# Kernel optimization log

Measured on AMD Instinct MI355X. Metric: run time of the kernel, lower is better.

## Reference

```python
import jax, jax.numpy as jnp
import numpy as np

EPS = 1e-5
V, D, S, B, H, DH, FF, LE, LD = 32000, 512, 1024, 2, 8, 64, 2048, 2, 2


def _ln(x, g, b):
    m = x.mean(-1, keepdims=True)
    v = ((x - m) ** 2).mean(-1, keepdims=True)
    return (x - m) * jax.lax.rsqrt(v + EPS) * g + b


def _mha(qi, ki, vi, wq, wk, wv, uw, ub, mask):
    # wq/wk/wv: [H, D, DH] stacked per-head no-bias projections (concat order == head order)
    q = jnp.einsum('bsd,hde->bhse', qi, wq)
    k = jnp.einsum('btd,hde->bhte', ki, wk)
    v = jnp.einsum('btd,hde->bhte', vi, wv)
    scale = float(wq.shape[-1]) ** 0.5  # FAITHFUL to source: scores are MULTIPLIED by sqrt(d_head)
    s = jnp.einsum('bhse,bhte->bhst', q, k) * scale
    s = jnp.where(mask, s, -jnp.inf)  # causal tril mask applied in every attention (incl. cross)
    a = jax.nn.softmax(s, axis=-1)
    o = jnp.einsum('bhst,bhte->bhse', a, v)
    b_, h_, s_, e_ = o.shape
    o = o.transpose(0, 2, 1, 3).reshape(b_, s_, h_ * e_)
    return o @ uw + ub


def _posenc(seq, d):
    pos = jnp.arange(seq, dtype=jnp.float32)[:, None]
    den = jnp.exp(jnp.arange(0, d, 2, dtype=jnp.float32) * (-np.log(10000.0) / d))
    pe = jnp.zeros((seq, d), jnp.float32)
    pe = pe.at[:, 0::2].set(jnp.sin(pos * den))
    pe = pe.at[:, 1::2].set(jnp.cos(pos * den))
    return pe


def _forward(tokens, emb, enc_wq, enc_wk, enc_wv, enc_uo_w, enc_uo_b,
             enc_ln1_g, enc_ln1_b, enc_ln2_g, enc_ln2_b,
             enc_ff_w1, enc_ff_b1, enc_ff_w2, enc_ff_b2,
             dec_sa_wq, dec_sa_wk, dec_sa_wv, dec_sa_uo_w, dec_sa_uo_b,
             dec_ca_wq, dec_ca_wk, dec_ca_wv, dec_ca_uo_w, dec_ca_uo_b,
             dec_ln1_g, dec_ln1_b, dec_ln2_g, dec_ln2_b, dec_ln3_g, dec_ln3_b,
             dec_ff_w1, dec_ff_b1, dec_ff_w2, dec_ff_b2,
             ln_enc_g, ln_enc_b, ln_dec_g, ln_dec_b, head_w, head_b):
    b, s = tokens.shape
    d = emb.shape[1]
    x = emb[tokens] + _posenc(s, d)  # [B, S, D]
    mask = jnp.tril(jnp.ones((s, s), bool))
    enc = jax.lax.stop_gradient(x)  # source: x.detach().clone()
    for l in range(enc_wq.shape[0]):
        h = _ln(enc, enc_ln1_g[l], enc_ln1_b[l])
        enc = enc + _mha(h, h, h, enc_wq[l], enc_wk[l], enc_wv[l], enc_uo_w[l], enc_uo_b[l], mask)
        h = _ln(enc, enc_ln2_g[l], enc_ln2_b[l])
        enc = enc + (jnp.maximum(h @ enc_ff_w1[l] + enc_ff_b1[l], 0.0) @ enc_ff_w2[l] + enc_ff_b2[l])
    enc = _ln(enc, ln_enc_g, ln_enc_b)
    for l in range(dec_sa_wq.shape[0]):
        h = _ln(x, dec_ln1_g[l], dec_ln1_b[l])
        x = x + _mha(h, h, h, dec_sa_wq[l], dec_sa_wk[l], dec_sa_wv[l], dec_sa_uo_w[l], dec_sa_uo_b[l], mask)
        h = _ln(x, dec_ln2_g[l], dec_ln2_b[l])
        x = x + _mha(h, enc, enc, dec_ca_wq[l], dec_ca_wk[l], dec_ca_wv[l], dec_ca_uo_w[l], dec_ca_uo_b[l], mask)
        h = _ln(x, dec_ln3_g[l], dec_ln3_b[l])
        x = x + (jnp.maximum(h @ dec_ff_w1[l] + dec_ff_b1[l], 0.0) @ dec_ff_w2[l] + dec_ff_b2[l])
    x = _ln(x, ln_dec_g, ln_dec_b)
    return x @ head_w + head_b  # [B, S, V]


def setup_inputs():
    key = jax.random.key(0)
    ks = iter(jax.random.split(key, 64))
    def n(shape):
        return jax.random.normal(next(ks), shape, jnp.float32) * 0.02
    return {
        'tokens': jax.random.randint(next(ks), (B, S), 0, V, jnp.int32),
        'emb': n((V, D)),
        'enc_wq': n((LE, H, D, DH)), 'enc_wk': n((LE, H, D, DH)), 'enc_wv': n((LE, H, D, DH)),
        'enc_uo_w': n((LE, D, D)), 'enc_uo_b': jnp.zeros((LE, D), jnp.float32),
        'enc_ln1_g': jnp.ones((LE, D), jnp.float32), 'enc_ln1_b': jnp.zeros((LE, D), jnp.float32),
        'enc_ln2_g': jnp.ones((LE, D), jnp.float32), 'enc_ln2_b': jnp.zeros((LE, D), jnp.float32),
        'enc_ff_w1': n((LE, D, FF)), 'enc_ff_b1': jnp.zeros((LE, FF), jnp.float32),
        'enc_ff_w2': n((LE, FF, D)), 'enc_ff_b2': jnp.zeros((LE, D), jnp.float32),
        'dec_sa_wq': n((LD, H, D, DH)), 'dec_sa_wk': n((LD, H, D, DH)), 'dec_sa_wv': n((LD, H, D, DH)),
        'dec_sa_uo_w': n((LD, D, D)), 'dec_sa_uo_b': jnp.zeros((LD, D), jnp.float32),
        'dec_ca_wq': n((LD, H, D, DH)), 'dec_ca_wk': n((LD, H, D, DH)), 'dec_ca_wv': n((LD, H, D, DH)),
        'dec_ca_uo_w': n((LD, D, D)), 'dec_ca_uo_b': jnp.zeros((LD, D), jnp.float32),
        'dec_ln1_g': jnp.ones((LD, D), jnp.float32), 'dec_ln1_b': jnp.zeros((LD, D), jnp.float32),
        'dec_ln2_g': jnp.ones((LD, D), jnp.float32), 'dec_ln2_b': jnp.zeros((LD, D), jnp.float32),
        'dec_ln3_g': jnp.ones((LD, D), jnp.float32), 'dec_ln3_b': jnp.zeros((LD, D), jnp.float32),
        'dec_ff_w1': n((LD, D, FF)), 'dec_ff_b1': jnp.zeros((LD, FF), jnp.float32),
        'dec_ff_w2': n((LD, FF, D)), 'dec_ff_b2': jnp.zeros((LD, D), jnp.float32),
        'ln_enc_g': jnp.ones((D,), jnp.float32), 'ln_enc_b': jnp.zeros((D,), jnp.float32),
        'ln_dec_g': jnp.ones((D,), jnp.float32), 'ln_dec_b': jnp.zeros((D,), jnp.float32),
        'head_w': n((D, V)), 'head_b': jnp.zeros((V,), jnp.float32),
    }


def reference(tokens, emb, enc_wq, enc_wk, enc_wv, enc_uo_w, enc_uo_b,
              enc_ln1_g, enc_ln1_b, enc_ln2_g, enc_ln2_b,
              enc_ff_w1, enc_ff_b1, enc_ff_w2, enc_ff_b2,
              dec_sa_wq, dec_sa_wk, dec_sa_wv, dec_sa_uo_w, dec_sa_uo_b,
              dec_ca_wq, dec_ca_wk, dec_ca_wv, dec_ca_uo_w, dec_ca_uo_b,
              dec_ln1_g, dec_ln1_b, dec_ln2_g, dec_ln2_b, dec_ln3_g, dec_ln3_b,
              dec_ff_w1, dec_ff_b1, dec_ff_w2, dec_ff_b2,
              ln_enc_g, ln_enc_b, ln_dec_g, ln_dec_b, head_w, head_b):
    return _forward(tokens, emb, enc_wq, enc_wk, enc_wv, enc_uo_w, enc_uo_b,
                    enc_ln1_g, enc_ln1_b, enc_ln2_g, enc_ln2_b,
                    enc_ff_w1, enc_ff_b1, enc_ff_w2, enc_ff_b2,
                    dec_sa_wq, dec_sa_wk, dec_sa_wv, dec_sa_uo_w, dec_sa_uo_b,
                    dec_ca_wq, dec_ca_wk, dec_ca_wv, dec_ca_uo_w, dec_ca_uo_b,
                    dec_ln1_g, dec_ln1_b, dec_ln2_g, dec_ln2_b, dec_ln3_g, dec_ln3_b,
                    dec_ff_w1, dec_ff_b1, dec_ff_w2, dec_ff_b2,
                    ln_enc_g, ln_enc_b, ln_dec_g, ln_dec_b, head_w, head_b)
```

## Files before the change

### kernel.cpp

```cpp
#include <hip/hip_runtime.h>
#include <cstddef>
#include <cstdint>

constexpr int Vv = 32000, Dd = 512, Ss = 1024, Bb = 2, Hh = 8, DHd = 64, FFf = 2048;
constexpr int Tt = Bb * Ss;
constexpr int QKVW = 3 * Dd;
constexpr float EPSf = 1e-5f;

typedef unsigned short ushort_t;
typedef short bf16x8 __attribute__((ext_vector_type(8)));
typedef short short4v __attribute__((ext_vector_type(4)));
typedef float f32x4 __attribute__((ext_vector_type(4)));

constexpr size_t AQKV = 0;
constexpr size_t AUO  = 4718592;
constexpr size_t AFF1 = 6291456;
constexpr size_t AFF2 = 10485760;
constexpr size_t AEND = 14680064;

__device__ __forceinline__ ushort_t f2b(float f) {
  unsigned int u = __float_as_uint(f);
  unsigned int r = (u + 0x7FFFu + ((u >> 16) & 1u)) >> 16;
  return (ushort_t)r;
}
__device__ __forceinline__ float bits2f(ushort_t u) {
  return __uint_as_float((unsigned int)u << 16);
}

__device__ __forceinline__ void st_out(float* p, float v) { *p = v; }
__device__ __forceinline__ void st_out(ushort_t* p, float v) { *p = f2b(v); }

__device__ __forceinline__ void gload_lds16(const void* g, void* l) {
  __builtin_amdgcn_global_load_lds(
      (const __attribute__((address_space(1))) unsigned int*)g,
      (__attribute__((address_space(3))) unsigned int*)l, 16, 0, 0);
}

__global__ __launch_bounds__(256) void embed_pe_k(const int* __restrict__ tok,
                                                  const float* __restrict__ emb,
                                                  float* __restrict__ X,
                                                  float* __restrict__ ENC) {
  int row = blockIdx.x;
  int s = row & (Ss - 1);
  int t = tok[row];
  const float* e = emb + (size_t)t * Dd;
  for (int d = threadIdx.x; d < Dd; d += 256) {
    int i = d >> 1;
    float den = expf(-(float)(2 * i) * (9.210340371976184f / 512.0f));
    float ang = (float)s * den;
    float pe = (d & 1) ? cosf(ang) : sinf(ang);
    float v = e[d] + pe;
    X[(size_t)row * Dd + d] = v;
    ENC[(size_t)row * Dd + d] = v;
  }
}

__global__ __launch_bounds__(256) void layernorm_k(const float* __restrict__ in,
                                                   const float* __restrict__ g,
                                                   const float* __restrict__ b,
                                                   ushort_t* __restrict__ out) {
  int row = blockIdx.x;
  const float* x = in + (size_t)row * Dd;
  int tid = threadIdx.x;
  float v0 = x[tid], v1 = x[tid + 256];
  float s = v0 + v1, ss = v0 * v0 + v1 * v1;
  for (int o = 32; o; o >>= 1) {
    s  += __shfl_down(s, o, 64);
    ss += __shfl_down(ss, o, 64);
  }
  __shared__ float rs[4], rss[4];
  int wid = tid >> 6, lane = tid & 63;
  if (lane == 0) { rs[wid] = s; rss[wid] = ss; }
  __syncthreads();
  __shared__ float mean_s, inv_s;
  if (tid == 0) {
    float a = rs[0] + rs[1] + rs[2] + rs[3];
    float c = rss[0] + rss[1] + rss[2] + rss[3];
    float m = a / Dd;
    float var = c / Dd - m * m;
    mean_s = m;
    inv_s = rsqrtf(var + EPSf);
  }
  __syncthreads();
  float m = mean_s, inv = inv_s;
  out[(size_t)row * Dd + tid]       = f2b((v0 - m) * inv * g[tid]       + b[tid]);
  out[(size_t)row * Dd + tid + 256] = f2b((v1 - m) * inv * g[tid + 256] + b[tid + 256]);
}

__global__ __launch_bounds__(256) void prep_all_k(
    const float* __restrict__ ewq, const float* __restrict__ ewk, const float* __restrict__ ewv,
    const float* __restrict__ swq, const float* __restrict__ swk, const float* __restrict__ swv,
    const float* __restrict__ cwq, const float* __restrict__ cwk, const float* __restrict__ cwv,
    const float* __restrict__ euo, const float* __restrict__ suo, const float* __restrict__ cuo,
    const float* __restrict__ eff1, const float* __restrict__ dff1,
    const float* __restrict__ eff2, const float* __restrict__ dff2,
    ushort_t* __restrict__ arena) {
  const float* src;
  ushort_t* dst;
  int R, C, tile;
  int idx = blockIdx.x;
  if (idx < 4608) {
    tile = idx & 31;
    int rest = idx >> 5;
    int h = rest & 7; rest >>= 3;
    int t = rest % 3, gl = rest / 3;
    int g = gl >> 1, l = gl & 1;
    const float* bq = (g == 0) ? ewq : (g == 1) ? swq : cwq;
    const float* bk = (g == 0) ? ewk : (g == 1) ? swk : cwk;
    const float* bv = (g == 0) ? ewv : (g == 1) ? swv : cwv;
    const float* base = (t == 0) ? bq : (t == 1) ? bk : bv;
    src = base + (size_t)l * (Hh * Dd * DHd) + (size_t)h * (Dd * DHd);
    dst = arena + AQKV + (size_t)gl * (QKVW * Dd) + ((size_t)t * Dd + h * DHd) * Dd;
    R = 512; C = 64;
  } else if (idx < 6144) {
    int i2 = idx - 4608;
    tile = i2 & 255;
    int gl = i2 >> 8;
    int g = gl >> 1, l = gl & 1;
    const float* base = (g == 0) ? euo : (g == 1) ? suo : cuo;
    src = base + (size_t)l * (Dd * Dd);
    dst = arena + AUO + (size_t)gl * (Dd * Dd);
    R = 512; C = 512;
  } else if (idx < 10240) {
    int i3 = idx - 6144;
    tile = i3 & 1023;
    int dl = i3 >> 10;
    int d = dl >> 1, l = dl & 1;
    src = (d ? dff1 : eff1) + (size_t)l * (Dd * FFf);
    dst = arena + AFF1 + (size_t)dl * (Dd * FFf);
    R = 512; C = 2048;
  } else {
    int i4 = idx - 10240;
    tile = i4 & 1023;
    int dl = i4 >> 10;
    int d = dl >> 1, l = dl & 1;
    src = (d ? dff2 : eff2) + (size_t)l * (FFf * Dd);
    dst = arena + AFF2 + (size_t)dl * (FFf * Dd);
    R = 2048; C = 512;
  }
  int nR = R >> 5;
  int r0 = (tile % nR) * 32, c0 = (tile / nR) * 32;
  __shared__ float tb[32][33];
  int tx = threadIdx.x & 31, ty = threadIdx.x >> 5;
#pragma unroll
  for (int i = 0; i < 4; i++)
    tb[ty + i * 8][tx] = src[(size_t)(r0 + ty + i * 8) * C + c0 + tx];
  __syncthreads();
#pragma unroll
  for (int i = 0; i < 4; i++)
    dst[(size_t)(c0 + ty + i * 8) * R + r0 + tx] = f2b(tb[tx][ty + i * 8]);
}

__global__ __launch_bounds__(256) void tcast_k(const float* __restrict__ in,
                                               ushort_t* __restrict__ out,
                                               int R, int C) {
  __shared__ float t[32][33];
  int c0 = blockIdx.x * 32, r0 = blockIdx.y * 32;
  int tx = threadIdx.x & 31, ty = threadIdx.x >> 5;
#pragma unroll
  for (int i = 0; i < 4; i++)
    t[ty + i * 8][tx] = in[(size_t)(r0 + ty + i * 8) * C + c0 + tx];
  __syncthreads();
#pragma unroll
  for (int i = 0; i < 4; i++)
    out[(size_t)(c0 + ty + i * 8) * R + r0 + tx] = f2b(t[tx][ty + i * 8]);
}

__device__ __forceinline__ void block_coords(bool nmajor, int nbM, int nbN,
                                             int& bmOut, int& bnOut) {
  int o = blockIdx.x;
  int nwg = gridDim.x;
  int q = nwg >> 3, r = nwg & 7;
  int x = o & 7, i = o >> 3;
  int l = (x < r ? x * (q + 1) : r * (q + 1) + (x - r) * q) + i;
  int mb, nb;
  if (nmajor) { mb = l % nbM; nb = l / nbM; }
  else        { nb = l % nbN; mb = l / nbN; }
  bmOut = mb; bnOut = nb;
}

template <int BM, int BN, bool NMAJOR, typename OutT, bool RELU>
__global__ __launch_bounds__(256) void gemm_bt_k(const ushort_t* __restrict__ A,
                                                 const ushort_t* __restrict__ BT,
                                                 const float* __restrict__ bias,
                                                 const float* __restrict__ resid,
                                                 OutT* __restrict__ C,
                                                 int M, int N, int K, int ldc,
                                                 int nbM, int nbN) {
  constexpr int FM = BM / 32, FN = BN / 32;
  __shared__ __align__(16) ushort_t As[2][BM * 64];
  __shared__ __align__(16) ushort_t Bs[2][BN * 64];

  int mb, nb;
  block_coords(NMAJOR, nbM, nbN, mb, nb);
  int bm = mb * BM, bn = nb * BN;

  int tid = threadIdx.x;
  int lane = tid & 63, w = tid >> 6;
  int wr = w >> 1, wc = w & 1;
  f32x4 acc[FM][FN];
#pragma unroll
  for (int m = 0; m < FM; m++)
#pragma unroll
    for (int n = 0; n < FN; n++) acc[m][n] = (f32x4){0.f, 0.f, 0.f, 0.f};

  const ushort_t* aBase = A + (size_t)bm * K;
  const ushort_t* bBase = BT + (size_t)bn * K;
  int lr = lane & 15;
  int lk = (lane >> 4) * 8;

  auto stage = [&](int buf, int k0) {
#pragma unroll
    for (int it = 0; it < BM / 32; it++) {
      int cid = it * 256 + tid;
      int row = cid >> 3, c8 = cid & 7;
      int sc8 = c8 ^ (row & 7);
      gload_lds16(aBase + (size_t)row * K + k0 + sc8 * 8, &As[buf][cid * 8]);
    }
#pragma unroll
    for (int it = 0; it < BN / 32; it++) {
      int cid = it * 256 + tid;
      int row = cid >> 3, c8 = cid & 7;
      int sc8 = c8 ^ (row & 7);
      gload_lds16(bBase + (size_t)row * K + k0 + sc8 * 8, &Bs[buf][cid * 8]);
    }
  };

  stage(0, 0);
  __syncthreads();
  int nt = K >> 6;
  for (int t = 0; t < nt; t++) {
    int cur = t & 1;
    if (t + 1 < nt) stage(cur ^ 1, (t + 1) << 6);
#pragma unroll
    for (int kk = 0; kk < 64; kk += 32) {
      bf16x8 af[FM], bfr[FN];
#pragma unroll
      for (int m = 0; m < FM; m++) {
        int row = wr * (BM / 2) + m * 16 + lr;
        af[m] = *(const bf16x8*)&As[cur][row * 64 + ((kk + lk) ^ ((row & 7) << 3))];
      }
#pragma unroll
      for (int n = 0; n < FN; n++) {
        int row = wc * (BN / 2) + n * 16 + lr;
        bfr[n] = *(const bf16x8*)&Bs[cur][row * 64 + ((kk + lk) ^ ((row & 7) << 3))];
      }
#pragma unroll
      for (int m = 0; m < FM; m++)
#pragma unroll
        for (int n = 0; n < FN; n++)
          acc[m][n] = __builtin_amdgcn_mfma_f32_16x16x32_bf16(af[m], bfr[n], acc[m][n], 0, 0, 0);
    }
    __syncthreads();
  }

  int rowg = (lane >> 4) * 4;
#pragma unroll
  for (int m = 0; m < FM; m++) {
    int row0 = bm + wr * (BM / 2) + m * 16 + rowg;
#pragma unroll
    for (int n = 0; n < FN; n++) {
      int col = bn + wc * (BN / 2) + n * 16 + lr;
      float bv = bias ? bias[col] : 0.0f;
#pragma unroll
      for (int rr = 0; rr < 4; rr++) {
        int row = row0 + rr;
        float v = acc[m][n][rr] + bv;
        if (resid) v += resid[(size_t)row * ldc + col];
        if (RELU)  v = fmaxf(v, 0.0f);
        st_out(&C[(size_t)row * ldc + col], v);
      }
    }
  }
}

__global__ __launch_bounds__(128) void fattn_k(const float* __restrict__ QKV,
                                               ushort_t* __restrict__ AO) {
  int bid = blockIdx.x;
  int i4 = bid >> 4;
  int qt = (i4 < 16) ? (31 - i4) : (i4 - 16);
  int h  = bid & 7;
  int b  = (bid >> 3) & 1;
  int q0 = qt * 32;
  int tid = threadIdx.x;
  int lane = tid & 63, w = tid >> 6;
  int g = lane >> 4, c = lane & 15;

  __shared__ __align__(16) ushort_t Qh[32 * 64], Ql[32 * 64];
  __shared__ __align__(16) ushort_t Kh[64 * 64], Kl[64 * 64];
  __shared__ __align__(16) ushort_t VT[64 * 64];
  __shared__ __align__(16) ushort_t Ps[2][16 * 64];

  {
    int row = tid >> 2, c0 = (tid & 3) * 16;
    const float* qb = QKV + ((size_t)(b * Ss + q0 + row) * QKVW + h * DHd + c0);
#pragma unroll
    for (int ii = 0; ii < 4; ii++) {
      float4 v = *(const float4*)(qb + ii * 4);
      int col = c0 + ii * 4;
      int sc = col ^ ((row & 7) << 3);
      ushort_t h0 = f2b(v.x), h1 = f2b(v.y), h2 = f2b(v.z), h3 = f2b(v.w);
      short4v hv = {(short)h0, (short)h1, (short)h2, (short)h3};
      short4v lv = {(short)f2b(v.x - bits2f(h0)), (short)f2b(v.y - bits2f(h1)),
                    (short)f2b(v.z - bits2f(h2)), (short)f2b(v.w - bits2f(h3))};
      *(short4v*)&Qh[row * 64 + sc] = hv;
      *(short4v*)&Ql[row * 64 + sc] = lv;
    }
  }

  f32x4 Oa[4];
#pragma unroll
  for (int n = 0; n < 4; n++) Oa[n] = (f32x4){0.f, 0.f, 0.f, 0.f};
  float mrow[4] = {-INFINITY, -INFINITY, -INFINITY, -INFINITY};
  float lrow[4] = {0.f, 0.f, 0.f, 0.f};

  int nkv = (qt >> 1) + 1;
  for (int it = 0; it < nkv; it++) {
    int t0 = it * 64;
    __syncthreads();
    {
      int row = tid >> 1, c0 = (tid & 1) * 32;
      const float* kb = QKV + ((size_t)(b * Ss + t0 + row) * QKVW + Dd + h * DHd + c0);
      const float* vb = kb + Dd;
#pragma unroll
      for (int ii = 0; ii < 8; ii++) {
        float4 v = *(const float4*)(kb + ii * 4);
        int col = c0 + ii * 4;
        int sc = col ^ ((row & 7) << 3);
        ushort_t h0 = f2b(v.x), h1 = f2b(v.y), h2 = f2b(v.z), h3 = f2b(v.w);
        short4v hv = {(short)h0, (short)h1, (short)h2, (short)h3};
        short4v lv = {(short)f2b(v.x - bits2f(h0)), (short)f2b(v.y - bits2f(h1)),
                      (short)f2b(v.z - bits2f(h2)), (short)f2b(v.w - bits2f(h3))};
        *(short4v*)&Kh[row * 64 + sc] = hv;
        *(short4v*)&Kl[row * 64 + sc] = lv;
      }
#pragma unroll
      for (int ii = 0; ii < 8; ii++) {
        float4 v = *(const float4*)(vb + ii * 4);
        int e0 = c0 + ii * 4;
        VT[(e0 + 0) * 64 + (row ^ (((e0 + 0) & 7) << 3))] = f2b(v.x);
        VT[(e0 + 1) * 64 + (row ^ (((e0 + 1) & 7) << 3))] = f2b(v.y);
        VT[(e0 + 2) * 64 + (row ^ (((e0 + 2) & 7) << 3))] = f2b(v.z);
        VT[(e0 + 3) * 64 + (row ^ (((e0 + 3) & 7) << 3))] = f2b(v.w);
      }
    }
    __syncthreads();

    int arow = w * 16 + c;
    int ksw0 = (0 + g * 8) ^ ((c & 7) << 3);
    int ksw1 = (32 + g * 8) ^ ((c & 7) << 3);
    bf16x8 qh0 = *(const bf16x8*)&Qh[arow * 64 + ksw0];
    bf16x8 qh1 = *(const bf16x8*)&Qh[arow * 64 + ksw1];
    bf16x8 ql0 = *(const bf16x8*)&Ql[arow * 64 + ksw0];
    bf16x8 ql1 = *(const bf16x8*)&Ql[arow * 64 + ksw1];

    f32x4 sfr[4];
#pragma unroll
    for (int n = 0; n < 4; n++) {
      int brow = n * 16 + c;
      bf16x8 kh0 = *(const bf16x8*)&Kh[brow * 64 + ksw0];
      bf16x8 kh1 = *(const bf16x8*)&Kh[brow * 64 + ksw1];
      bf16x8 kl0 = *(const bf16x8*)&Kl[brow * 64 + ksw0];
      bf16x8 kl1 = *(const bf16x8*)&Kl[brow * 64 + ksw1];
      f32x4 a = (f32x4){0.f, 0.f, 0.f, 0.f};
      a = __builtin_amdgcn_mfma_f32_16x16x32_bf16(qh0, kl0, a, 0, 0, 0);
      a = __builtin_amdgcn_mfma_f32_16x16x32_bf16(qh1, kl1, a, 0, 0, 0);
      a = __builtin_amdgcn_mfma_f32_16x16x32_bf16(ql0, kh0, a, 0, 0, 0);
      a = __builtin_amdgcn_mfma_f32_16x16x32_bf16(ql1, kh1, a, 0, 0, 0);
      a = __builtin_amdgcn_mfma_f32_16x16x32_bf16(qh0, kh0, a, 0, 0, 0);
      a = __builtin_amdgcn_mfma_f32_16x16x32_bf16(qh1, kh1, a, 0, 0, 0);
      sfr[n] = a;
    }

#pragma unroll
    for (int n = 0; n < 4; n++) {
#pragma unroll
      for (int rr = 0; rr < 4; rr++) sfr[n][rr] *= 8.0f;
    }
    if (it == nkv - 1) {
#pragma unroll
      for (int n = 0; n < 4; n++) {
        int t = t0 + n * 16 + c;
#pragma unroll
        for (int rr = 0; rr < 4; rr++) {
          int s = q0 + w * 16 + g * 4 + rr;
          if (t > s) sfr[n][rr] = -INFINITY;
        }
      }
    }

    float pnew[4], scold[4];
#pragma unroll
    for (int rr = 0; rr < 4; rr++) {
      float tm = fmaxf(fmaxf(sfr[0][rr], sfr[1][rr]), fmaxf(sfr[2][rr], sfr[3][rr]));
      tm = fmaxf(tm, __shfl_xor(tm, 1));
      tm = fmaxf(tm, __shfl_xor(tm, 2));
      tm = fmaxf(tm, __shfl_xor(tm, 4));
      tm = fmaxf(tm, __shfl_xor(tm, 8));
      float mn = fmaxf(mrow[rr], tm);
      scold[rr] = __expf(mrow[rr] - mn);
      mrow[rr] = mn;
      pnew[rr] = mn;
    }
#pragma unroll
    for (int n = 0; n < 4; n++) {
#pragma unroll
      for (int rr = 0; rr < 4; rr++) sfr[n][rr] = __expf(sfr[n][rr] - pnew[rr]);
    }
#pragma unroll
    for (int rr = 0; rr < 4; rr++) {
      float s = sfr[0][rr] + sfr[1][rr] + sfr[2][rr] + sfr[3][rr];
      s += __shfl_xor(s, 1);
      s += __shfl_xor(s, 2);
      s += __shfl_xor(s, 4);
      s += __shfl_xor(s, 8);
      lrow[rr] = lrow[rr] * scold[rr] + s;
    }

#pragma unroll
    for (int n = 0; n < 4; n++) {
#pragma unroll
      for (int rr = 0; rr < 4; rr++) {
        int prow = g * 4 + rr;
        Ps[w][prow * 64 + ((n * 16 + c) ^ ((prow & 7) << 3))] = f2b(sfr[n][rr]);
      }
    }

#pragma unroll
    for (int n = 0; n < 4; n++) {
#pragma unroll
      for (int rr = 0; rr < 4; rr++) Oa[n][rr] *= scold[rr];
    }

    bf16x8 pa0 = *(const bf16x8*)&Ps[w][c * 64 + ksw0];
    bf16x8 pa1 = *(const bf16x8*)&Ps[w][c * 64 + ksw1];
#pragma unroll
    for (int n = 0; n < 4; n++) {
      int vrow = n * 16 + c;
      bf16x8 v0 = *(const bf16x8*)&VT[vrow * 64 + ksw0];
      bf16x8 v1 = *(const bf16x8*)&VT[vrow * 64 + ksw1];
      Oa[n] = __builtin_amdgcn_mfma_f32_16x16x32_bf16(pa0, v0, Oa[n], 0, 0, 0);
      Oa[n] = __builtin_amdgcn_mfma_f32_16x16x32_bf16(pa1, v1, Oa[n], 0, 0, 0);
    }
  }

#pragma unroll
  for (int rr = 0; rr < 4; rr++) {
    float inv = 1.0f / lrow[rr];
    int row = b * Ss + q0 + w * 16 + g * 4 + rr;
#pragma unroll
    for (int n = 0; n < 4; n++) {
      AO[(size_t)row * Dd + h * DHd + n * 16 + c] = f2b(Oa[n][rr] * inv);
    }
  }
}

template <int BM, int BN, bool NMAJOR, typename OutT, bool RELU>
static void gemm_bt(hipStream_t st, const ushort_t* A, const ushort_t* BT, const float* bias,
                    const float* resid, OutT* C, int M, int N, int K, int ldc) {
  int nbM = M / BM, nbN = N / BN;
  dim3 g(nbM * nbN), blk(256);
  gemm_bt_k<BM, BN, NMAJOR, OutT, RELU><<<g, blk, 0, st>>>(A, BT, bias, resid, C, M, N, K, ldc, nbM, nbN);
}

extern "C" void kernel_launch(void* const* d_in, const int* in_sizes, int n_in,
                              void* d_out, int out_size, void* d_ws, size_t ws_size,
                              hipStream_t stream) {
  const int*   tokens    = (const int*)d_in[0];
  const float* emb       = (const float*)d_in[1];
  const float* enc_wq    = (const float*)d_in[2];
  const float* enc_wk    = (const float*)d_in[3];
  const float* enc_wv    = (const float*)d_in[4];
  const float* enc_uo_w  = (const float*)d_in[5];
  const float* enc_uo_b  = (const float*)d_in[6];
  const float* enc_ln1_g = (const float*)d_in[7];
  const float* enc_ln1_b = (const float*)d_in[8];
  const float* enc_ln2_g = (const float*)d_in[9];
  const float* enc_ln2_b = (const float*)d_in[10];
  const float* enc_ff_w1 = (const float*)d_in[11];
  const float* enc_ff_b1 = (const float*)d_in[12];
  const float* enc_ff_w2 = (const float*)d_in[13];
  const float* enc_ff_b2 = (const float*)d_in[14];
  const float* dec_sa_wq = (const float*)d_in[15];
  const float* dec_sa_wk = (const float*)d_in[16];
  const float* dec_sa_wv = (const float*)d_in[17];
  const float* dec_sa_uo_w = (const float*)d_in[18];
  const float* dec_sa_uo_b = (const float*)d_in[19];
  const float* dec_ca_wq = (const float*)d_in[20];
  const float* dec_ca_wk = (const float*)d_in[21];
  const float* dec_ca_wv = (const float*)d_in[22];
  const float* dec_ca_uo_w = (const float*)d_in[23];
  const float* dec_ca_uo_b = (const float*)d_in[24];
  const float* dec_ln1_g = (const float*)d_in[25];
  const float* dec_ln1_b = (const float*)d_in[26];
  const float* dec_ln2_g = (const float*)d_in[27];
  const float* dec_ln2_b = (const float*)d_in[28];
  const float* dec_ln3_g = (const float*)d_in[29];
  const float* dec_ln3_b = (const float*)d_in[30];
  const float* dec_ff_w1 = (const float*)d_in[31];
  const float* dec_ff_b1 = (const float*)d_in[32];
  const float* dec_ff_w2 = (const float*)d_in[33];
  const float* dec_ff_b2 = (const float*)d_in[34];
  const float* ln_enc_g  = (const float*)d_in[35];
  const float* ln_enc_b  = (const float*)d_in[36];
  const float* ln_dec_g  = (const float*)d_in[37];
  const float* ln_dec_b  = (const float*)d_in[38];
  const float* head_w    = (const float*)d_in[39];
  const float* head_b    = (const float*)d_in[40];
  float* out = (float*)d_out;

  char* ws = (char*)d_ws;
  size_t off = 0;
  auto alloc = [&](size_t bytes) {
    void* p = ws + off;
    off += (bytes + 255) & ~(size_t)255;
    return p;
  };
  ushort_t* Hb    = (ushort_t*)alloc((size_t)Tt * Dd * 2);
  ushort_t* ENCFb = (ushort_t*)alloc((size_t)Tt * Dd * 2);
  float*    X     = (float*)alloc((size_t)Tt * Dd * 4);
  float*    ENC   = (float*)alloc((size_t)Tt * Dd * 4);
  float*    QKV   = (float*)alloc((size_t)Tt * QKVW * 4);
  ushort_t* AO    = (ushort_t*)alloc((size_t)Tt * Dd * 2);
  ushort_t* Fb    = (ushort_t*)alloc((size_t)Tt * FFf * 2);
  ushort_t* ARENA = (ushort_t*)alloc(AEND * 2);
  ushort_t* BThead = (ushort_t*)X;

  dim3 blk(256), fblk(128);
  dim3 attnG(Bb * Hh * (Ss / 32));

  prep_all_k<<<14336, blk, 0, stream>>>(
      enc_wq, enc_wk, enc_wv, dec_sa_wq, dec_sa_wk, dec_sa_wv,
      dec_ca_wq, dec_ca_wk, dec_ca_wv,
      enc_uo_w, dec_sa_uo_w, dec_ca_uo_w,
      enc_ff_w1, dec_ff_w1, enc_ff_w2, dec_ff_w2, ARENA);

  embed_pe_k<<<Tt, blk, 0, stream>>>(tokens, emb, X, ENC);

  for (int l = 0; l < 2; l++) {
    const ushort_t* BTq  = ARENA + AQKV + (size_t)(0 * 2 + l) * (QKVW * Dd);
    const ushort_t* BTu  = ARENA + AUO  + (size_t)(0 * 2 + l) * (Dd * Dd);
    const ushort_t* BT1  = ARENA + AFF1 + (size_t)(0 * 2 + l) * (Dd * FFf);
    const ushort_t* BT2  = ARENA + AFF2 + (size_t)(0 * 2 + l) * (FFf * Dd);
    layernorm_k<<<Tt, blk, 0, stream>>>(ENC, enc_ln1_g + l * Dd, enc_ln1_b + l * Dd, Hb);
    gemm_bt<64, 128, true, float, false>(stream, Hb, BTq, nullptr, nullptr, QKV, Tt, QKVW, Dd, QKVW);
    fattn_k<<<attnG, fblk, 0, stream>>>(QKV, AO);
    gemm_bt<64, 64, true, float, false>(stream, AO, BTu, enc_uo_b + l * Dd, ENC, ENC, Tt, Dd, Dd, Dd);
    layernorm_k<<<Tt, blk, 0, stream>>>(ENC, enc_ln2_g + l * Dd, enc_ln2_b + l * Dd, Hb);
    gemm_bt<128, 128, true, ushort_t, true>(stream, Hb, BT1, enc_ff_b1 + l * FFf, nullptr, Fb, Tt, FFf, Dd, FFf);
    gemm_bt<64, 64, false, float, false>(stream, Fb, BT2, enc_ff_b2 + l * Dd, ENC, ENC, Tt, Dd, FFf, Dd);
  }
  layernorm_k<<<Tt, blk, 0, stream>>>(ENC, ln_enc_g, ln_enc_b, ENCFb);

  for (int l = 0; l < 2; l++) {
    const ushort_t* BTsa = ARENA + AQKV + (size_t)(1 * 2 + l) * (QKVW * Dd);
    const ushort_t* BTca = ARENA + AQKV + (size_t)(2 * 2 + l) * (QKVW * Dd);
    const ushort_t* BTsu = ARENA + AUO  + (size_t)(1 * 2 + l) * (Dd * Dd);
    const ushort_t* BTcu = ARENA + AUO  + (size_t)(2 * 2 + l) * (Dd * Dd);
    const ushort_t* BT1  = ARENA + AFF1 + (size_t)(1 * 2 + l) * (Dd * FFf);
    const ushort_t* BT2  = ARENA + AFF2 + (size_t)(1 * 2 + l) * (FFf * Dd);
    layernorm_k<<<Tt, blk, 0, stream>>>(X, dec_ln1_g + l * Dd, dec_ln1_b + l * Dd, Hb);
    gemm_bt<64, 128, true, float, false>(stream, Hb, BTsa, nullptr, nullptr, QKV, Tt, QKVW, Dd, QKVW);
    fattn_k<<<attnG, fblk, 0, stream>>>(QKV, AO);
    gemm_bt<64, 64, true, float, false>(stream, AO, BTsu, dec_sa_uo_b + l * Dd, X, X, Tt, Dd, Dd, Dd);
    layernorm_k<<<Tt, blk, 0, stream>>>(X, dec_ln2_g + l * Dd, dec_ln2_b + l * Dd, Hb);
    gemm_bt<64, 64, true, float, false>(stream, Hb, BTca, nullptr, nullptr, QKV, Tt, Dd, Dd, QKVW);
    gemm_bt<64, 128, true, float, false>(stream, ENCFb, BTca + (size_t)Dd * Dd, nullptr, nullptr,
                                         QKV + Dd, Tt, 2 * Dd, Dd, QKVW);
    fattn_k<<<attnG, fblk, 0, stream>>>(QKV, AO);
    gemm_bt<64, 64, true, float, false>(stream, AO, BTcu, dec_ca_uo_b + l * Dd, X, X, Tt, Dd, Dd, Dd);
    layernorm_k<<<Tt, blk, 0, stream>>>(X, dec_ln3_g + l * Dd, dec_ln3_b + l * Dd, Hb);
    gemm_bt<128, 128, true, ushort_t, true>(stream, Hb, BT1, dec_ff_b1 + l * FFf, nullptr, Fb, Tt, FFf, Dd, FFf);
    gemm_bt<64, 64, false, float, false>(stream, Fb, BT2, dec_ff_b2 + l * Dd, X, X, Tt, Dd, FFf, Dd);
  }
  layernorm_k<<<Tt, blk, 0, stream>>>(X, ln_dec_g, ln_dec_b, Hb);

  tcast_k<<<dim3(Vv / 32, Dd / 32), blk, 0, stream>>>(head_w, BThead, Dd, Vv);
  gemm_bt<128, 128, true, float, false>(stream, Hb, BThead, head_b, nullptr, out, Tt, Vv, Dd, Vv);
}
```

Measured before the change: 825.0 us.

## Batch independent encoder and decoder stages into shared multi-problem launches

Reorders the schedule so that decoder layer 0 self-attention, which depends only on the embeddings, runs in the same launches as encoder layer 0. Layernorm, QKV GEMM, attention and output projection each process two problems per grid. Embedding and the head-weight transpose are folded into the weight-prep kernel, and the FF1 tile shrinks from 128x128 to 64x128. This cuts launch count and fills the GPU better at small grid sizes, at the cost of extra workspace buffers and one larger combined prep grid.

```diff
diff --git a/kernel.cpp b/kernel.cpp
--- a/kernel.cpp
+++ b/kernel.cpp
@@ -34,57 +34,6 @@
   __builtin_amdgcn_global_load_lds(
       (const __attribute__((address_space(1))) unsigned int*)g,
       (__attribute__((address_space(3))) unsigned int*)l, 16, 0, 0);
-}
-
-__global__ __launch_bounds__(256) void embed_pe_k(const int* __restrict__ tok,
-                                                  const float* __restrict__ emb,
-                                                  float* __restrict__ X,
-                                                  float* __restrict__ ENC) {
-  int row = blockIdx.x;
-  int s = row & (Ss - 1);
-  int t = tok[row];
-  const float* e = emb + (size_t)t * Dd;
-  for (int d = threadIdx.x; d < Dd; d += 256) {
-    int i = d >> 1;
-    float den = expf(-(float)(2 * i) * (9.210340371976184f / 512.0f));
-    float ang = (float)s * den;
-    float pe = (d & 1) ? cosf(ang) : sinf(ang);
-    float v = e[d] + pe;
-    X[(size_t)row * Dd + d] = v;
-    ENC[(size_t)row * Dd + d] = v;
-  }
-}
-
-__global__ __launch_bounds__(256) void layernorm_k(const float* __restrict__ in,
-                                                   const float* __restrict__ g,
-                                                   const float* __restrict__ b,
-                                                   ushort_t* __restrict__ out) {
-  int row = blockIdx.x;
-  const float* x = in + (size_t)row * Dd;
-  int tid = threadIdx.x;
-  float v0 = x[tid], v1 = x[tid + 256];
-  float s = v0 + v1, ss = v0 * v0 + v1 * v1;
-  for (int o = 32; o; o >>= 1) {
-    s  += __shfl_down(s, o, 64);
-    ss += __shfl_down(ss, o, 64);
-  }
-  __shared__ float rs[4], rss[4];
-  int wid = tid >> 6, lane = tid & 63;
-  if (lane == 0) { rs[wid] = s; rss[wid] = ss; }
-  __syncthreads();
-  __shared__ float mean_s, inv_s;
-  if (tid == 0) {
-    float a = rs[0] + rs[1] + rs[2] + rs[3];
-    float c = rss[0] + rss[1] + rss[2] + rss[3];
-    float m = a / Dd;
-    float var = c / Dd - m * m;
-    mean_s = m;
-    inv_s = rsqrtf(var + EPSf);
-  }
-  __syncthreads();
-  float m = mean_s, inv = inv_s;
-  out[(size_t)row * Dd + tid]       = f2b((v0 - m) * inv * g[tid]       + b[tid]);
-  out[(size_t)row * Dd + tid + 256] = f2b((v1 - m) * inv * g[tid + 256] + b[tid + 256]);
 }
 
 __global__ __launch_bounds__(256) void prep_all_k(
@@ -94,11 +43,32 @@
     const float* __restrict__ euo, const float* __restrict__ suo, const float* __restrict__ cuo,
     const float* __restrict__ eff1, const float* __restrict__ dff1,
     const float* __restrict__ eff2, const float* __restrict__ dff2,
-    ushort_t* __restrict__ arena) {
+    ushort_t* __restrict__ arena,
+    const int* __restrict__ tok, const float* __restrict__ emb,
+    float* __restrict__ X, float* __restrict__ ENC,
+    const float* __restrict__ headw, ushort_t* __restrict__ headDst) {
+  int idx = blockIdx.x;
+
+  if (idx >= 14336 && idx < 16384) {
+    int row = idx - 14336;
+    int s = row & (Ss - 1);
+    int t = tok[row];
+    const float* e = emb + (size_t)t * Dd;
+    for (int d = threadIdx.x; d < Dd; d += 256) {
+      int i = d >> 1;
+      float den = expf(-(float)(2 * i) * (9.210340371976184f / 512.0f));
+      float ang = (float)s * den;
+      float pe = (d & 1) ? cosf(ang) : sinf(ang);
+      float v = e[d] + pe;
+      X[(size_t)row * Dd + d] = v;
+      ENC[(size_t)row * Dd + d] = v;
+    }
+    return;
+  }
+
   const float* src;
   ushort_t* dst;
   int R, C, tile;
-  int idx = blockIdx.x;
   if (idx < 4608) {
     tile = idx & 31;
     int rest = idx >> 5;
@@ -129,7 +99,7 @@
     src = (d ? dff1 : eff1) + (size_t)l * (Dd * FFf);
     dst = arena + AFF1 + (size_t)dl * (Dd * FFf);
     R = 512; C = 2048;
-  } else {
+  } else if (idx < 14336) {
     int i4 = idx - 10240;
     tile = i4 & 1023;
     int dl = i4 >> 10;
@@ -137,6 +107,10 @@
     src = (d ? dff2 : eff2) + (size_t)l * (FFf * Dd);
     dst = arena + AFF2 + (size_t)dl * (FFf * Dd);
     R = 2048; C = 512;
+  } else {
+    tile = idx - 16384;
+    src = headw; dst = headDst;
+    R = 512; C = 32000;
   }
   int nR = R >> 5;
   int r0 = (tile % nR) * 32, c0 = (tile / nR) * 32;
@@ -166,10 +140,47 @@
     out[(size_t)(c0 + ty + i * 8) * R + r0 + tx] = f2b(t[tx][ty + i * 8]);
 }
 
-__device__ __forceinline__ void block_coords(bool nmajor, int nbM, int nbN,
-                                             int& bmOut, int& bnOut) {
-  int o = blockIdx.x;
-  int nwg = gridDim.x;
+__global__ __launch_bounds__(256) void ln2_k(const float* __restrict__ in0,
+                                             const float* __restrict__ g0,
+                                             const float* __restrict__ b0,
+                                             ushort_t* __restrict__ o0,
+                                             const float* __restrict__ in1,
+                                             const float* __restrict__ g1,
+                                             const float* __restrict__ b1,
+                                             ushort_t* __restrict__ o1,
+                                             int nblk0) {
+  int row = blockIdx.x;
+  const float* in = in0; const float* g = g0; const float* b = b0; ushort_t* out = o0;
+  if (row >= nblk0) { row -= nblk0; in = in1; g = g1; b = b1; out = o1; }
+  const float* x = in + (size_t)row * Dd;
+  int tid = threadIdx.x;
+  float v0 = x[tid], v1 = x[tid + 256];
+  float s = v0 + v1, ss = v0 * v0 + v1 * v1;
+  for (int o = 32; o; o >>= 1) {
+    s  += __shfl_down(s, o, 64);
+    ss += __shfl_down(ss, o, 64);
+  }
+  __shared__ float rs[4], rss[4];
+  int wid = tid >> 6, lane = tid & 63;
+  if (lane == 0) { rs[wid] = s; rss[wid] = ss; }
+  __syncthreads();
+  __shared__ float mean_s, inv_s;
+  if (tid == 0) {
+    float a = rs[0] + rs[1] + rs[2] + rs[3];
+    float c = rss[0] + rss[1] + rss[2] + rss[3];
+    float m = a / Dd;
+    float var = c / Dd - m * m;
+    mean_s = m;
+    inv_s = rsqrtf(var + EPSf);
+  }
+  __syncthreads();
+  float m = mean_s, inv = inv_s;
+  out[(size_t)row * Dd + tid]       = f2b((v0 - m) * inv * g[tid]       + b[tid]);
+  out[(size_t)row * Dd + tid + 256] = f2b((v1 - m) * inv * g[tid + 256] + b[tid + 256]);
+}
+
+__device__ __forceinline__ void block_coords(int o, int nwg, bool nmajor,
+                                             int nbM, int nbN, int& bmOut, int& bnOut) {
   int q = nwg >> 3, r = nwg & 7;
   int x = o & 7, i = o >> 3;
   int l = (x < r ? x * (q + 1) : r * (q + 1) + (x - r) * q) + i;
@@ -179,21 +190,25 @@
   bmOut = mb; bnOut = nb;
 }
 
+struct GD {
+  const ushort_t* A; const ushort_t* BT; const float* bias; const float* resid;
+  void* C; int N; int K; int ldc; int nbM; int nbN; int nwg;
+};
+
 template <int BM, int BN, bool NMAJOR, typename OutT, bool RELU>
-__global__ __launch_bounds__(256) void gemm_bt_k(const ushort_t* __restrict__ A,
-                                                 const ushort_t* __restrict__ BT,
-                                                 const float* __restrict__ bias,
-                                                 const float* __restrict__ resid,
-                                                 OutT* __restrict__ C,
-                                                 int M, int N, int K, int ldc,
-                                                 int nbM, int nbN) {
+__global__ __launch_bounds__(256) void gemm2_k(GD d0, GD d1, int nblk0) {
   constexpr int FM = BM / 32, FN = BN / 32;
   __shared__ __align__(16) ushort_t As[2][BM * 64];
   __shared__ __align__(16) ushort_t Bs[2][BN * 64];
 
+  GD d = d0;
+  int o = blockIdx.x;
+  if (o >= nblk0) { d = d1; o -= nblk0; }
   int mb, nb;
-  block_coords(NMAJOR, nbM, nbN, mb, nb);
+  block_coords(o, d.nwg, NMAJOR, d.nbM, d.nbN, mb, nb);
   int bm = mb * BM, bn = nb * BN;
+  int K = d.K, ldc = d.ldc;
+  OutT* C = (OutT*)d.C;
 
   int tid = threadIdx.x;
   int lane = tid & 63, w = tid >> 6;
@@ -204,8 +219,8 @@
 #pragma unroll
     for (int n = 0; n < FN; n++) acc[m][n] = (f32x4){0.f, 0.f, 0.f, 0.f};
 
-  const ushort_t* aBase = A + (size_t)bm * K;
-  const ushort_t* bBase = BT + (size_t)bn * K;
+  const ushort_t* aBase = d.A + (size_t)bm * K;
+  const ushort_t* bBase = d.BT + (size_t)bn * K;
   int lr = lane & 15;
   int lk = (lane >> 4) * 8;
 
@@ -261,12 +276,12 @@
 #pragma unroll
     for (int n = 0; n < FN; n++) {
       int col = bn + wc * (BN / 2) + n * 16 + lr;
-      float bv = bias ? bias[col] : 0.0f;
+      float bv = d.bias ? d.bias[col] : 0.0f;
 #pragma unroll
       for (int rr = 0; rr < 4; rr++) {
         int row = row0 + rr;
         float v = acc[m][n][rr] + bv;
-        if (resid) v += resid[(size_t)row * ldc + col];
+        if (d.resid) v += d.resid[(size_t)row * ldc + col];
         if (RELU)  v = fmaxf(v, 0.0f);
         st_out(&C[(size_t)row * ldc + col], v);
       }
@@ -274,9 +289,14 @@
   }
 }
 
-__global__ __launch_bounds__(128) void fattn_k(const float* __restrict__ QKV,
-                                               ushort_t* __restrict__ AO) {
+__global__ __launch_bounds__(128) void fattn_k(const float* __restrict__ QKV0,
+                                               ushort_t* __restrict__ AO0,
+                                               const float* __restrict__ QKV1,
+                                               ushort_t* __restrict__ AO1,
+                                               int nblk0) {
   int bid = blockIdx.x;
+  const float* QKV = QKV0; ushort_t* AO = AO0;
+  if (bid >= nblk0) { bid -= nblk0; QKV = QKV1; AO = AO1; }
   int i4 = bid >> 4;
   int qt = (i4 < 16) ? (31 - i4) : (i4 - 16);
   int h  = bid & 7;
@@ -455,12 +475,23 @@
   }
 }
 
+static GD mkGD(const ushort_t* A, const ushort_t* BT, const float* bias,
+               const float* resid, void* C, int M, int N, int K, int ldc,
+               int BM, int BN) {
+  GD d;
+  d.A = A; d.BT = BT; d.bias = bias; d.resid = resid; d.C = C;
+  d.N = N; d.K = K; d.ldc = ldc;
+  d.nbM = M / BM; d.nbN = N / BN; d.nwg = d.nbM * d.nbN;
+  return d;
+}
+
 template <int BM, int BN, bool NMAJOR, typename OutT, bool RELU>
-static void gemm_bt(hipStream_t st, const ushort_t* A, const ushort_t* BT, const float* bias,
-                    const float* resid, OutT* C, int M, int N, int K, int ldc) {
-  int nbM = M / BM, nbN = N / BN;
-  dim3 g(nbM * nbN), blk(256);
-  gemm_bt_k<BM, BN, NMAJOR, OutT, RELU><<<g, blk, 0, st>>>(A, BT, bias, resid, C, M, N, K, ldc, nbM, nbN);
+static void gemm1(hipStream_t st, GD d) {
+  gemm2_k<BM, BN, NMAJOR, OutT, RELU><<<dim3(d.nwg), dim3(256), 0, st>>>(d, d, d.nwg);
+}
+template <int BM, int BN, bool NMAJOR, typename OutT, bool RELU>
+static void gemm2(hipStream_t st, GD d0, GD d1) {
+  gemm2_k<BM, BN, NMAJOR, OutT, RELU><<<dim3(d0.nwg + d1.nwg), dim3(256), 0, st>>>(d0, d1, d0.nwg);
 }
 
 extern "C" void kernel_launch(void* const* d_in, const int* in_sizes, int n_in,
@@ -517,64 +548,101 @@
     return p;
   };
   ushort_t* Hb    = (ushort_t*)alloc((size_t)Tt * Dd * 2);
+  ushort_t* Hb2   = (ushort_t*)alloc((size_t)Tt * Dd * 2);
   ushort_t* ENCFb = (ushort_t*)alloc((size_t)Tt * Dd * 2);
   float*    X     = (float*)alloc((size_t)Tt * Dd * 4);
   float*    ENC   = (float*)alloc((size_t)Tt * Dd * 4);
   float*    QKV   = (float*)alloc((size_t)Tt * QKVW * 4);
+  float*    QKV2  = (float*)alloc((size_t)Tt * QKVW * 4);
   ushort_t* AO    = (ushort_t*)alloc((size_t)Tt * Dd * 2);
+  ushort_t* AO2   = (ushort_t*)alloc((size_t)Tt * Dd * 2);
   ushort_t* Fb    = (ushort_t*)alloc((size_t)Tt * FFf * 2);
   ushort_t* ARENA = (ushort_t*)alloc(AEND * 2);
-  ushort_t* BThead = (ushort_t*)X;
+
+  size_t headBytes = (size_t)Vv * Dd * 2;
+  bool headInPrep = (off + headBytes) <= ws_size;
+  ushort_t* BThead = headInPrep ? (ushort_t*)alloc(headBytes) : (ushort_t*)X;
 
   dim3 blk(256), fblk(128);
-  dim3 attnG(Bb * Hh * (Ss / 32));
-
-  prep_all_k<<<14336, blk, 0, stream>>>(
-      enc_wq, enc_wk, enc_wv, dec_sa_wq, dec_sa_wk, dec_sa_wv,
-      dec_ca_wq, dec_ca_wk, dec_ca_wv,
-      enc_uo_w, dec_sa_uo_w, dec_ca_uo_w,
-      enc_ff_w1, dec_ff_w1, enc_ff_w2, dec_ff_w2, ARENA);
-
-  embed_pe_k<<<Tt, blk, 0, stream>>>(tokens, emb, X, ENC);
+  int attnB = Bb * Hh * (Ss / 32);
+
+  {
+    int nprep = 14336 + 2048 + (headInPrep ? 16000 : 0);
+    prep_all_k<<<nprep, blk, 0, stream>>>(
+        enc_wq, enc_wk, enc_wv, dec_sa_wq, dec_sa_wk, dec_sa_wv,
+        dec_ca_wq, dec_ca_wk, dec_ca_wv,
+        enc_uo_w, dec_sa_uo_w, dec_ca_uo_w,
+        enc_ff_w1, dec_ff_w1, enc_ff_w2, dec_ff_w2, ARENA,
+        tokens, emb, X, ENC, head_w, headInPrep ? BThead : nullptr);
+  }
+
+  auto BTq  = [&](int gl) { return ARENA + AQKV + (size_t)gl * (QKVW * Dd); };
+  auto BTu  = [&](int gl) { return ARENA + AUO  + (size_t)gl * (Dd * Dd); };
+  auto BT1  = [&](int dl) { return ARENA + AFF1 + (size_t)dl * (Dd * FFf); };
+  auto BT2  = [&](int dl) { return ARENA + AFF2 + (size_t)dl * (FFf * Dd); };
+
+  ln2_k<<<2 * Tt, blk, 0, stream>>>(ENC, enc_ln1_g, enc_ln1_b, Hb,
+                                    X, dec_ln1_g, dec_ln1_b, Hb2, Tt);
+  gemm2<64, 128, true, float, false>(stream,
+      mkGD(Hb,  BTq(0), nullptr, nullptr, QKV,  Tt, QKVW, Dd, QKVW, 64, 128),
+      mkGD(Hb2, BTq(2), nullptr, nullptr, QKV2, Tt, QKVW, Dd, QKVW, 64, 128));
+  fattn_k<<<2 * attnB, fblk, 0, stream>>>(QKV, AO, QKV2, AO2, attnB);
+  gemm2<64, 64, true, float, false>(stream,
+      mkGD(AO,  BTu(0), enc_uo_b,    ENC, ENC, Tt, Dd, Dd, Dd, 64, 64),
+      mkGD(AO2, BTu(2), dec_sa_uo_b, X,   X,   Tt, Dd, Dd, Dd, 64, 64));
+  ln2_k<<<Tt, blk, 0, stream>>>(ENC, enc_ln2_g, enc_ln2_b, Hb, ENC, enc_ln2_g, enc_ln2_b, Hb, Tt);
+  gemm1<64, 128, true, ushort_t, true>(stream,
+      mkGD(Hb, BT1(0), enc_ff_b1, nullptr, Fb, Tt, FFf, Dd, FFf, 64, 128));
+  gemm1<64, 64, false, float, false>(stream,
+      mkGD(Fb, BT2(0), enc_ff_b2, ENC, ENC, Tt, Dd, FFf, Dd, 64, 64));
+
+  ln2_k<<<Tt, blk, 0, stream>>>(ENC, enc_ln1_g + Dd, enc_ln1_b + Dd, Hb,
+                                ENC, enc_ln1_g + Dd, enc_ln1_b + Dd, Hb, Tt);
+  gemm1<64, 128, true, float, false>(stream,
+      mkGD(Hb, BTq(1), nullptr, nullptr, QKV, Tt, QKVW, Dd, QKVW, 64, 128));
+  fattn_k<<<attnB, fblk, 0, stream>>>(QKV, AO, QKV, AO, attnB);
+  gemm1<64, 64, true, float, false>(stream,
+      mkGD(AO, BTu(1), enc_uo_b + Dd, ENC, ENC, Tt, Dd, Dd, Dd, 64, 64));
+  ln2_k<<<Tt, blk, 0, stream>>>(ENC, enc_ln2_g + Dd, enc_ln2_b + Dd, Hb,
+                                ENC, enc_ln2_g + Dd, enc_ln2_b + Dd, Hb, Tt);
+  gemm1<64, 128, true, ushort_t, true>(stream,
+      mkGD(Hb, BT1(1), enc_ff_b1 + FFf, nullptr, Fb, Tt, FFf, Dd, FFf, 64, 128));
+  gemm1<64, 64, false, float, false>(stream,
+      mkGD(Fb, BT2(1), enc_ff_b2 + Dd, ENC, ENC, Tt, Dd, FFf, Dd, 64, 64));
 
   for (int l = 0; l < 2; l++) {
-    const ushort_t* BTq  = ARENA + AQKV + (size_t)(0 * 2 + l) * (QKVW * Dd);
-    const ushort_t* BTu  = ARENA + AUO  + (size_t)(0 * 2 + l) * (Dd * Dd);
-    const ushort_t* BT1  = ARENA + AFF1 + (size_t)(0 * 2 + l) * (Dd * FFf);
-    const ushort_t* BT2  = ARENA + AFF2 + (size_t)(0 * 2 + l) * (FFf * Dd);
-    layernorm_k<<<Tt, blk, 0, stream>>>(ENC, enc_ln1_g + l * Dd, enc_ln1_b + l * Dd, Hb);
-    gemm_bt<64, 128, true, float, false>(stream, Hb, BTq, nullptr, nullptr, QKV, Tt, QKVW, Dd, QKVW);
-    fattn_k<<<attnG, fblk, 0, stream>>>(QKV, AO);
-    gemm_bt<64, 64, true, float, false>(stream, AO, BTu, enc_uo_b + l * Dd, ENC, ENC, Tt, Dd, Dd, Dd);
-    layernorm_k<<<Tt, blk, 0, stream>>>(ENC, enc_ln2_g + l * Dd, enc_ln2_b + l * Dd, Hb);
-    gemm_bt<128, 128, true, ushort_t, true>(stream, Hb, BT1, enc_ff_b1 + l * FFf, nullptr, Fb, Tt, FFf, Dd, FFf);
-    gemm_bt<64, 64, false, float, false>(stream, Fb, BT2, enc_ff_b2 + l * Dd, ENC, ENC, Tt, Dd, FFf, Dd);
-  }
-  layernorm_k<<<Tt, blk, 0, stream>>>(ENC, ln_enc_g, ln_enc_b, ENCFb);
-
-  for (int l = 0; l < 2; l++) {
-    const ushort_t* BTsa = ARENA + AQKV + (size_t)(1 * 2 + l) * (QKVW * Dd);
-    const ushort_t* BTca = ARENA + AQKV + (size_t)(2 * 2 + l) * (QKVW * Dd);
-    const ushort_t* BTsu = ARENA + AUO  + (size_t)(1 * 2 + l) * (Dd * Dd);
-    const ushort_t* BTcu = ARENA + AUO  + (size_t)(2 * 2 + l) * (Dd * Dd);
-    const ushort_t* BT1  = ARENA + AFF1 + (size_t)(1 * 2 + l) * (Dd * FFf);
-    const ushort_t* BT2  = ARENA + AFF2 + (size_t)(1 * 2 + l) * (FFf * Dd);
-    layernorm_k<<<Tt, blk, 0, stream>>>(X, dec_ln1_g + l * Dd, dec_ln1_b + l * Dd, Hb);
-    gemm_bt<64, 128, true, float, false>(stream, Hb, BTsa, nullptr, nullptr, QKV, Tt, QKVW, Dd, QKVW);
-    fattn_k<<<attnG, fblk, 0, stream>>>(QKV, AO);
-    gemm_bt<64, 64, true, float, false>(stream, AO, BTsu, dec_sa_uo_b + l * Dd, X, X, Tt, Dd, Dd, Dd);
-    layernorm_k<<<Tt, blk, 0, stream>>>(X, dec_ln2_g + l * Dd, dec_ln2_b + l * Dd, Hb);
-    gemm_bt<64, 64, true, float, false>(stream, Hb, BTca, nullptr, nullptr, QKV, Tt, Dd, Dd, QKVW);
-    gemm_bt<64, 128, true, float, false>(stream, ENCFb, BTca + (size_t)Dd * Dd, nullptr, nullptr,
-                                         QKV + Dd, Tt, 2 * Dd, Dd, QKVW);
-    fattn_k<<<attnG, fblk, 0, stream>>>(QKV, AO);
-    gemm_bt<64, 64, true, float, false>(stream, AO, BTcu, dec_ca_uo_b + l * Dd, X, X, Tt, Dd, Dd, Dd);
-    layernorm_k<<<Tt, blk, 0, stream>>>(X, dec_ln3_g + l * Dd, dec_ln3_b + l * Dd, Hb);
-    gemm_bt<128, 128, true, ushort_t, true>(stream, Hb, BT1, dec_ff_b1 + l * FFf, nullptr, Fb, Tt, FFf, Dd, FFf);
-    gemm_bt<64, 64, false, float, false>(stream, Fb, BT2, dec_ff_b2 + l * Dd, X, X, Tt, Dd, FFf, Dd);
-  }
-  layernorm_k<<<Tt, blk, 0, stream>>>(X, ln_dec_g, ln_dec_b, Hb);
-
-  tcast_k<<<dim3(Vv / 32, Dd / 32), blk, 0, stream>>>(head_w, BThead, Dd, Vv);
-  gemm_bt<128, 128, true, float, false>(stream, Hb, BThead, head_b, nullptr, out, Tt, Vv, Dd, Vv);
-}
+    if (l == 0) {
+      ln2_k<<<2 * Tt, blk, 0, stream>>>(ENC, ln_enc_g, ln_enc_b, ENCFb,
+                                        X, dec_ln2_g, dec_ln2_b, Hb, Tt);
+    } else {
+      ln2_k<<<Tt, blk, 0, stream>>>(X, dec_ln1_g + Dd, dec_ln1_b + Dd, Hb,
+                                    X, dec_ln1_g + Dd, dec_ln1_b + Dd, Hb, Tt);
+      gemm1<64, 128, true, float, false>(stream,
+          mkGD(Hb, BTq(3), nullptr, nullptr, QKV, Tt, QKVW, Dd, QKVW, 64, 128));
+      fattn_k<<<attnB, fblk, 0, stream>>>(QKV, AO, QKV, AO, attnB);
+      gemm1<64, 64, true, float, false>(stream,
+          mkGD(AO, BTu(3), dec_sa_uo_b + Dd, X, X, Tt, Dd, Dd, Dd, 64, 64));
+      ln2_k<<<Tt, blk, 0, stream>>>(X, dec_ln2_g + Dd, dec_ln2_b + Dd, Hb,
+                                    X, dec_ln2_g + Dd, dec_ln2_b + Dd, Hb, Tt);
+    }
+    const ushort_t* BTca = BTq(4 + l);
+    gemm2<64, 128, true, float, false>(stream,
+        mkGD(Hb,    BTca,                    nullptr, nullptr, QKV,      Tt, Dd,     Dd, QKVW, 64, 128),
+        mkGD(ENCFb, BTca + (size_t)Dd * Dd,  nullptr, nullptr, QKV + Dd, Tt, 2 * Dd, Dd, QKVW, 64, 128));
+    fattn_k<<<attnB, fblk, 0, stream>>>(QKV, AO, QKV, AO, attnB);
+    gemm1<64, 64, true, float, false>(stream,
+        mkGD(AO, BTu(4 + l), dec_ca_uo_b + l * Dd, X, X, Tt, Dd, Dd, Dd, 64, 64));
+    ln2_k<<<Tt, blk, 0, stream>>>(X, dec_ln3_g + l * Dd, dec_ln3_b + l * Dd, Hb,
+                                  X, dec_ln3_g + l * Dd, dec_ln3_b + l * Dd, Hb, Tt);
+    gemm1<64, 128, true, ushort_t, true>(stream,
+        mkGD(Hb, BT1(2 + l), dec_ff_b1 + l * FFf, nullptr, Fb, Tt, FFf, Dd, FFf, 64, 128));
+    gemm1<64, 64, false, float, false>(stream,
+        mkGD(Fb, BT2(2 + l), dec_ff_b2 + l * Dd, X, X, Tt, Dd, FFf, Dd, 64, 64));
+  }
+  ln2_k<<<Tt, blk, 0, stream>>>(X, ln_dec_g, ln_dec_b, Hb, X, ln_dec_g, ln_dec_b, Hb, Tt);
+
+  if (!headInPrep)
+    tcast_k<<<dim3(Vv / 32, Dd / 32), blk, 0, stream>>>(head_w, BThead, Dd, Vv);
+  gemm1<128, 128, true, float, false>(stream,
+      mkGD(Hb, BThead, head_b, nullptr, out, Tt, Vv, Dd, Vv, 128, 128));
+}
```

Result: faster. 759.3 us (-8.0%).
